# Performance work log

Hardware: AMD Instinct MI355X
Metric: run time of the kernel (lower is better)

## Reference

```python
import jax, jax.numpy as jnp
import numpy as np

NBIT = 4          # weight bit-width
GROUP_SIZE = 128  # weight quantization group size (divides k)
HAS_WEIGHT_ZEROS = True


def _quant_dequant_weights(w, group_size=GROUP_SIZE, nbit=NBIT, has_zeros=HAS_WEIGHT_ZEROS):
    # Mirrors torchao _quantize + quantize_per_channel_group, then dequantizes
    # (the native kernel dequantizes inline with the matmul; math is identical).
    qmin = -(1 << (nbit - 1))
    qmax = (1 << (nbit - 1)) - 1
    n, k = w.shape
    g = w.reshape(-1, group_size)                      # [n*k/gs, gs]
    vmin = g.min(axis=1, keepdims=True)
    vmax = g.max(axis=1, keepdims=True)
    scales = (vmax - vmin) / (qmax - qmin)             # per-group scale
    if has_zeros:
        zeros = qmin - jnp.round(vmin / scales)
    else:
        zeros = jnp.zeros_like(scales)
    q = jnp.clip(jnp.round(g / scales) + zeros, qmin, qmax)
    deq = (q - zeros) * scales
    return deq.reshape(n, k)


def _dyn_quant_dequant_act(x):
    # Dynamic per-token (per-row) asymmetric int8 activation quantization.
    qmin, qmax = -128, 127
    xmin = x.min(axis=-1, keepdims=True)
    xmax = x.max(axis=-1, keepdims=True)
    scale = (xmax - xmin) / (qmax - qmin)
    zero = qmin - jnp.round(xmin / scale)
    q = jnp.clip(jnp.round(x / scale) + zero, qmin, qmax)
    return (q - zero) * scale


def setup_inputs() -> dict:
    key = jax.random.key(0)
    k1, k2 = jax.random.split(key)
    x = jax.random.normal(k1, (4, 2048, 4096), dtype=jnp.float32)
    weights = jax.random.normal(k2, (4096, 4096), dtype=jnp.float32) * 0.02
    return {"x": x, "weights": weights}


def reference(x, weights):
    w_deq = _quant_dequant_weights(weights)            # [n, k]
    x_deq = _dyn_quant_dequant_act(x)                  # [..., m, k]
    # y[..., m, n] = x_deq @ w_deq^T
    return jnp.einsum('bmk,nk->bmn', x_deq, w_deq)
```

## Files before the change

kernel.cpp:

```cpp
#include <hip/hip_runtime.h>
#include <hip/hip_bf16.h>
#include <cfloat>

typedef __attribute__((ext_vector_type(8))) short bf16x8;
typedef __attribute__((ext_vector_type(4))) float f32x4;

#define M_DIM 8192
#define N_DIM 4096
#define K_DIM 4096

__device__ inline ushort f2bf(float f) {
    unsigned u = __float_as_uint(f);
    unsigned r = (u + 0x7FFFu + ((u >> 16) & 1u)) >> 16;
    return (ushort)r;
}

#define SWZ(x) ((x) ^ ((((x) >> 7) & 7) << 4))

__global__ __launch_bounds__(256) void w_dequant(const float* __restrict__ w,
                                                 ushort* __restrict__ wq) {
    int g = blockIdx.x * 4 + (threadIdx.x >> 6);
    int lane = threadIdx.x & 63;
    const float* src = w + (size_t)g * 128;
    float2 v = *(const float2*)(src + lane * 2);
    float mn = fminf(v.x, v.y), mx = fmaxf(v.x, v.y);
#pragma unroll
    for (int s = 1; s < 64; s <<= 1) {
        mn = fminf(mn, __shfl_xor(mn, s));
        mx = fmaxf(mx, __shfl_xor(mx, s));
    }
    float scale = (mx - mn) / 15.0f;
    float zero  = -8.0f - rintf(mn / scale);
    float q0 = fminf(fmaxf(rintf(v.x / scale) + zero, -8.0f), 7.0f);
    float q1 = fminf(fmaxf(rintf(v.y / scale) + zero, -8.0f), 7.0f);
    ushort2 o;
    o.x = f2bf((q0 - zero) * scale);
    o.y = f2bf((q1 - zero) * scale);
    *(ushort2*)(wq + (size_t)g * 128 + lane * 2) = o;
}

__global__ __launch_bounds__(256) void act_qdq(const float* __restrict__ x,
                                               ushort* __restrict__ xq) {
    __shared__ float smn[4], smx[4];
    int row = blockIdx.x;
    const float* xr = x + (size_t)row * K_DIM;
    ushort* xo = xq + (size_t)row * K_DIM;
    int t = threadIdx.x;
    float4 v[4];
    float mn = FLT_MAX, mx = -FLT_MAX;
#pragma unroll
    for (int i = 0; i < 4; i++) {
        v[i] = ((const float4*)xr)[t + i * 256];
        mn = fminf(mn, fminf(fminf(v[i].x, v[i].y), fminf(v[i].z, v[i].w)));
        mx = fmaxf(mx, fmaxf(fmaxf(v[i].x, v[i].y), fmaxf(v[i].z, v[i].w)));
    }
#pragma unroll
    for (int s = 1; s < 64; s <<= 1) {
        mn = fminf(mn, __shfl_xor(mn, s));
        mx = fmaxf(mx, __shfl_xor(mx, s));
    }
    int w = t >> 6;
    if ((t & 63) == 0) { smn[w] = mn; smx[w] = mx; }
    __syncthreads();
    mn = fminf(fminf(smn[0], smn[1]), fminf(smn[2], smn[3]));
    mx = fmaxf(fmaxf(smx[0], smx[1]), fmaxf(smx[2], smx[3]));
    float scale = (mx - mn) / 255.0f;
    float zero  = -128.0f - rintf(mn / scale);
#pragma unroll
    for (int i = 0; i < 4; i++) {
        float e0 = v[i].x, e1 = v[i].y, e2 = v[i].z, e3 = v[i].w;
        ushort4 o;
        float q;
        q = fminf(fmaxf(rintf(e0 / scale) + zero, -128.0f), 127.0f); o.x = f2bf((q - zero) * scale);
        q = fminf(fmaxf(rintf(e1 / scale) + zero, -128.0f), 127.0f); o.y = f2bf((q - zero) * scale);
        q = fminf(fmaxf(rintf(e2 / scale) + zero, -128.0f), 127.0f); o.z = f2bf((q - zero) * scale);
        q = fminf(fmaxf(rintf(e3 / scale) + zero, -128.0f), 127.0f); o.w = f2bf((q - zero) * scale);
        ((ushort4*)xo)[t + i * 256] = o;
    }
}

#define BM 256
#define BN 256
#define BK 64
#define NT (K_DIM / BK)

__global__ __launch_bounds__(512, 1) void gemm_bt8(const ushort* __restrict__ A,
                                                   const ushort* __restrict__ B,
                                                   float* __restrict__ C) {
    __shared__ __align__(16) ushort As[2][BM * BK];
    __shared__ __align__(16) ushort Bs[2][BN * BK];

    const int nbx = N_DIM / BN;
    const int nwg = (M_DIM / BM) * nbx;
    int bid = blockIdx.x;
    bid = (bid & 7) * (nwg / 8) + (bid >> 3);
    int mb = bid / nbx, nb = bid % nbx;
    size_t m0 = (size_t)mb * BM, n0 = (size_t)nb * BN;

    const int t = threadIdx.x;
    const int w = t >> 6, lane = t & 63;
    const int wm = w >> 2, wn = w & 3;
    const int lr = lane & 15;
    const int lk = (lane >> 4) << 3;

    const ushort* Ab = A + m0 * K_DIM;
    const ushort* Bb = B + n0 * K_DIM;

    auto STAGE = [&](int T, int qq) {
        if (T >= NT) return;
        int d = T & 1;
        bool isA = qq < 4;
        int rq = isA ? qq : qq - 4;
        ushort* reg = isA ? As[d] : Bs[d];
        const ushort* gbase = isA ? Ab : Bb;
        int base = rq * 8192 + w * 1024;
        int lb = base + lane * 16;
        int lg = SWZ(lb);
        int r = lg >> 7;
        int c = (lg & 127) >> 1;
        __builtin_amdgcn_global_load_lds(
            (const __attribute__((address_space(1))) unsigned int*)(gbase + (size_t)r * K_DIM + T * BK + c),
            (__attribute__((address_space(3))) unsigned int*)((char*)reg + base),
            16, 0, 0);
    };

    f32x4 acc[8][4] = {};
    bf16x8 afr[2][2], bfr[4][2];

#define PHASE(d, q, sT1, sq1, sT2, sq2, vm) do {                                  \
    if ((q) == 0) {                                                               \
        _Pragma("unroll") for (int ni = 0; ni < 4; ni++)                          \
        _Pragma("unroll") for (int kk = 0; kk < 2; kk++) {                        \
            int row = wn * 64 + ni * 16 + lr;                                     \
            int lg = row * 128 + (kk * 32 + lk) * 2;                              \
            int pb = SWZ(lg);                                                     \
            bfr[ni][kk] = *(const bf16x8*)((const char*)Bs[d] + pb);              \
        }                                                                         \
    }                                                                             \
    _Pragma("unroll") for (int ii = 0; ii < 2; ii++)                              \
    _Pragma("unroll") for (int kk = 0; kk < 2; kk++) {                            \
        int row = (q) * 64 + wm * 32 + ii * 16 + lr;                              \
        int lg = row * 128 + (kk * 32 + lk) * 2;                                  \
        int pb = SWZ(lg);                                                         \
        afr[ii][kk] = *(const bf16x8*)((const char*)As[d] + pb);                  \
    }                                                                             \
    STAGE(sT1, sq1);                                                              \
    STAGE(sT2, sq2);                                                              \
    __builtin_amdgcn_s_barrier();                                                 \
    asm volatile("s_waitcnt lgkmcnt(0)" ::: "memory");                            \
    __builtin_amdgcn_sched_barrier(0);                                            \
    __builtin_amdgcn_s_setprio(1);                                                \
    _Pragma("unroll") for (int ii = 0; ii < 2; ii++)                              \
    _Pragma("unroll") for (int ni = 0; ni < 4; ni++)                              \
    _Pragma("unroll") for (int kk = 0; kk < 2; kk++)                              \
        acc[(q) * 2 + ii][ni] = __builtin_amdgcn_mfma_f32_16x16x32_bf16(          \
            afr[ii][kk], bfr[ni][kk], acc[(q) * 2 + ii][ni], 0, 0, 0);            \
    __builtin_amdgcn_s_setprio(0);                                                \
    if ((vm) == 1) asm volatile("s_waitcnt vmcnt(8)" ::: "memory");               \
    if ((vm) == 2) asm volatile("s_waitcnt vmcnt(0)" ::: "memory");               \
    __builtin_amdgcn_s_barrier();                                                 \
  } while (0)

    STAGE(0, 0); STAGE(0, 1); STAGE(0, 2); STAGE(0, 3);
    STAGE(0, 4); STAGE(0, 5); STAGE(0, 6); STAGE(0, 7);
    STAGE(1, 4); STAGE(1, 5); STAGE(1, 6); STAGE(1, 7);
    STAGE(1, 0); STAGE(1, 1);
    asm volatile("s_waitcnt vmcnt(6)" ::: "memory");
    __builtin_amdgcn_s_barrier();

#pragma unroll 1
    for (int i = 0; i < NT / 2 - 1; i++) {
        int T0 = 2 * i;
        PHASE(0, 0, T0 + 1, 2, T0 + 1, 3, 1);
        PHASE(0, 1, T0 + 2, 4, T0 + 2, 5, 1);
        PHASE(0, 2, T0 + 2, 6, T0 + 2, 7, 1);
        PHASE(0, 3, T0 + 2, 0, T0 + 2, 1, 1);
        PHASE(1, 0, T0 + 2, 2, T0 + 2, 3, 1);
        PHASE(1, 1, T0 + 3, 4, T0 + 3, 5, 1);
        PHASE(1, 2, T0 + 3, 6, T0 + 3, 7, 1);
        PHASE(1, 3, T0 + 3, 0, T0 + 3, 1, 1);
    }

    PHASE(0, 0, NT - 1, 2, NT - 1, 3, 1);
    PHASE(0, 1, NT, 0, NT, 0, 1);
    PHASE(0, 2, NT, 0, NT, 0, 1);
    PHASE(0, 3, NT, 0, NT, 0, 2);
    PHASE(1, 0, NT, 0, NT, 0, 0);
    PHASE(1, 1, NT, 0, NT, 0, 0);
    PHASE(1, 2, NT, 0, NT, 0, 0);
    PHASE(1, 3, NT, 0, NT, 0, 0);
#undef PHASE

    int fq = lane >> 4;
#pragma unroll
    for (int mi = 0; mi < 8; mi++) {
#pragma unroll
        for (int ni = 0; ni < 4; ni++) {
#pragma unroll
            for (int r = 0; r < 4; r++) {
                size_t crow = m0 + (mi >> 1) * 64 + wm * 32 + (mi & 1) * 16 + fq * 4 + r;
                C[crow * N_DIM + n0 + wn * 64 + ni * 16 + lr] = acc[mi][ni][r];
            }
        }
    }
}

extern "C" void kernel_launch(void* const* d_in, const int* in_sizes, int n_in,
                              void* d_out, int out_size, void* d_ws, size_t ws_size,
                              hipStream_t stream) {
    const float* x = (const float*)d_in[0];
    const float* w = (const float*)d_in[1];
    float* out = (float*)d_out;

    ushort* wq = (ushort*)d_ws;
    ushort* xq = (ushort*)((char*)d_ws + (size_t)N_DIM * K_DIM * 2);

    hipLaunchKernelGGL(w_dequant, dim3((N_DIM * K_DIM / 128) / 4), dim3(256), 0, stream, w, wq);
    hipLaunchKernelGGL(act_qdq, dim3(M_DIM), dim3(256), 0, stream, x, xq);
    hipLaunchKernelGGL(gemm_bt8, dim3((M_DIM / BM) * (N_DIM / BN)), dim3(512), 0, stream, xq, wq, out);
}
```

Baseline: 327.1 us.

## Double-buffer register fragments to overlap LDS reads with MFMA compute

Register fragments for A and B become double-buffered, so each phase runs its MFMAs on fragments already in registers while loading the next phase's fragments from LDS. One barrier per phase is removed and the vmcnt wait thresholds are retuned to match the new ordering of global-to-LDS stages. The intent is to hide LDS read latency behind matrix math. In exchange it uses more VGPRs, which could lower occupancy, and the changed wait counts risk read-after-write hazards on the LDS buffers.

```diff
diff --git a/kernel.cpp b/kernel.cpp
--- a/kernel.cpp
+++ b/kernel.cpp
@@ -125,40 +125,42 @@
     };
 
     f32x4 acc[8][4] = {};
-    bf16x8 afr[2][2], bfr[4][2];
-
-#define PHASE(d, q, sT1, sq1, sT2, sq2, vm) do {                                  \
-    if ((q) == 0) {                                                               \
-        _Pragma("unroll") for (int ni = 0; ni < 4; ni++)                          \
-        _Pragma("unroll") for (int kk = 0; kk < 2; kk++) {                        \
-            int row = wn * 64 + ni * 16 + lr;                                     \
-            int lg = row * 128 + (kk * 32 + lk) * 2;                              \
-            int pb = SWZ(lg);                                                     \
-            bfr[ni][kk] = *(const bf16x8*)((const char*)Bs[d] + pb);              \
-        }                                                                         \
-    }                                                                             \
+    bf16x8 afr[2][2][2];
+    bf16x8 bfr[2][4][2];
+
+#define LOADA(S, d, q) do {                                                       \
     _Pragma("unroll") for (int ii = 0; ii < 2; ii++)                              \
     _Pragma("unroll") for (int kk = 0; kk < 2; kk++) {                            \
         int row = (q) * 64 + wm * 32 + ii * 16 + lr;                              \
         int lg = row * 128 + (kk * 32 + lk) * 2;                                  \
-        int pb = SWZ(lg);                                                         \
-        afr[ii][kk] = *(const bf16x8*)((const char*)As[d] + pb);                  \
-    }                                                                             \
+        afr[S][ii][kk] = *(const bf16x8*)((const char*)As[d] + SWZ(lg));          \
+    } } while (0)
+#define LOADB(S, d) do {                                                          \
+    _Pragma("unroll") for (int ni = 0; ni < 4; ni++)                              \
+    _Pragma("unroll") for (int kk = 0; kk < 2; kk++) {                            \
+        int row = wn * 64 + ni * 16 + lr;                                         \
+        int lg = row * 128 + (kk * 32 + lk) * 2;                                  \
+        bfr[S][ni][kk] = *(const bf16x8*)((const char*)Bs[d] + SWZ(lg));          \
+    } } while (0)
+
+#define PHASE(q, SA, SB, SN, dn, qn, sT1, sq1, sT2, sq2, vm) do {                 \
+    __builtin_amdgcn_s_setprio(1);                                                \
+    _Pragma("unroll") for (int kk = 0; kk < 2; kk++)                              \
+    _Pragma("unroll") for (int ii = 0; ii < 2; ii++)                              \
+    _Pragma("unroll") for (int ni = 0; ni < 4; ni++)                              \
+        acc[(q) * 2 + ii][ni] = __builtin_amdgcn_mfma_f32_16x16x32_bf16(          \
+            afr[SA][ii][kk], bfr[SB][ni][kk], acc[(q) * 2 + ii][ni], 0, 0, 0);    \
+    __builtin_amdgcn_s_setprio(0);                                                \
+    if ((qn) == 0) LOADB(dn, dn);                                                 \
+    LOADA(SN, dn, qn);                                                            \
     STAGE(sT1, sq1);                                                              \
     STAGE(sT2, sq2);                                                              \
-    __builtin_amdgcn_s_barrier();                                                 \
     asm volatile("s_waitcnt lgkmcnt(0)" ::: "memory");                            \
-    __builtin_amdgcn_sched_barrier(0);                                            \
-    __builtin_amdgcn_s_setprio(1);                                                \
-    _Pragma("unroll") for (int ii = 0; ii < 2; ii++)                              \
-    _Pragma("unroll") for (int ni = 0; ni < 4; ni++)                              \
-    _Pragma("unroll") for (int kk = 0; kk < 2; kk++)                              \
-        acc[(q) * 2 + ii][ni] = __builtin_amdgcn_mfma_f32_16x16x32_bf16(          \
-            afr[ii][kk], bfr[ni][kk], acc[(q) * 2 + ii][ni], 0, 0, 0);            \
-    __builtin_amdgcn_s_setprio(0);                                                \
-    if ((vm) == 1) asm volatile("s_waitcnt vmcnt(8)" ::: "memory");               \
+    if ((vm) == 0) asm volatile("s_waitcnt vmcnt(6)" ::: "memory");               \
+    if ((vm) == 1) asm volatile("s_waitcnt vmcnt(2)" ::: "memory");               \
     if ((vm) == 2) asm volatile("s_waitcnt vmcnt(0)" ::: "memory");               \
     __builtin_amdgcn_s_barrier();                                                 \
+    __builtin_amdgcn_sched_barrier(0);                                            \
   } while (0)
 
     STAGE(0, 0); STAGE(0, 1); STAGE(0, 2); STAGE(0, 3);
@@ -167,29 +169,35 @@
     STAGE(1, 0); STAGE(1, 1);
     asm volatile("s_waitcnt vmcnt(6)" ::: "memory");
     __builtin_amdgcn_s_barrier();
+    LOADB(0, 0);
+    LOADA(0, 0, 0);
+    asm volatile("s_waitcnt lgkmcnt(0)" ::: "memory");
+    __builtin_amdgcn_sched_barrier(0);
 
 #pragma unroll 1
     for (int i = 0; i < NT / 2 - 1; i++) {
         int T0 = 2 * i;
-        PHASE(0, 0, T0 + 1, 2, T0 + 1, 3, 1);
-        PHASE(0, 1, T0 + 2, 4, T0 + 2, 5, 1);
-        PHASE(0, 2, T0 + 2, 6, T0 + 2, 7, 1);
-        PHASE(0, 3, T0 + 2, 0, T0 + 2, 1, 1);
-        PHASE(1, 0, T0 + 2, 2, T0 + 2, 3, 1);
-        PHASE(1, 1, T0 + 3, 4, T0 + 3, 5, 1);
-        PHASE(1, 2, T0 + 3, 6, T0 + 3, 7, 1);
-        PHASE(1, 3, T0 + 3, 0, T0 + 3, 1, 1);
-    }
-
-    PHASE(0, 0, NT - 1, 2, NT - 1, 3, 1);
-    PHASE(0, 1, NT, 0, NT, 0, 1);
-    PHASE(0, 2, NT, 0, NT, 0, 1);
-    PHASE(0, 3, NT, 0, NT, 0, 2);
-    PHASE(1, 0, NT, 0, NT, 0, 0);
-    PHASE(1, 1, NT, 0, NT, 0, 0);
-    PHASE(1, 2, NT, 0, NT, 0, 0);
-    PHASE(1, 3, NT, 0, NT, 0, 0);
+        PHASE(0, 0, 0, 1, 0, 1, T0 + 1, 2, T0 + 1, 3, 0);
+        PHASE(1, 1, 0, 0, 0, 2, T0 + 2, 4, T0 + 2, 5, 0);
+        PHASE(2, 0, 0, 1, 0, 3, T0 + 2, 6, T0 + 2, 7, 0);
+        PHASE(3, 1, 0, 0, 1, 0, T0 + 2, 0, T0 + 2, 1, 0);
+        PHASE(0, 0, 1, 1, 1, 1, T0 + 2, 2, T0 + 2, 3, 0);
+        PHASE(1, 1, 1, 0, 1, 2, T0 + 3, 4, T0 + 3, 5, 0);
+        PHASE(2, 0, 1, 1, 1, 3, T0 + 3, 6, T0 + 3, 7, 0);
+        PHASE(3, 1, 1, 0, 0, 0, T0 + 3, 0, T0 + 3, 1, 0);
+    }
+
+    PHASE(0, 0, 0, 1, 0, 1, NT - 1, 2, NT - 1, 3, 0);
+    PHASE(1, 1, 0, 0, 0, 2, NT, 0, NT, 0, 1);
+    PHASE(2, 0, 0, 1, 0, 3, NT, 0, NT, 0, 2);
+    PHASE(3, 1, 0, 0, 1, 0, NT, 0, NT, 0, 3);
+    PHASE(0, 0, 1, 1, 1, 1, NT, 0, NT, 0, 3);
+    PHASE(1, 1, 1, 0, 1, 2, NT, 0, NT, 0, 3);
+    PHASE(2, 0, 1, 1, 1, 3, NT, 0, NT, 0, 3);
+    PHASE(3, 1, 1, 0, 0, 0, NT, 0, NT, 0, 3);
 #undef PHASE
+#undef LOADA
+#undef LOADB
 
     int fq = lane >> 4;
 #pragma unroll
```

Result: no change. 324.3 us (-0.9%).
